# Performance work log

Hardware: AMD Instinct MI355X
Metric: run time of the kernel (lower is better)

Reference implementation:

```python
import jax, jax.numpy as jnp
import numpy as np

C = 512
NUM_GROUPS = 32
EPS = 1e-6


def setup_inputs() -> dict:
    key = jax.random.key(0)
    ks = jax.random.split(key, 10)
    B, H, W = 4, 64, 64
    scale = 1.0 / np.sqrt(C)
    return {
        "hidden_states": jax.random.normal(ks[0], (B, C, H, W), dtype=jnp.float32),
        "gn_scale": jnp.ones((C,), dtype=jnp.float32),
        "gn_bias": jnp.zeros((C,), dtype=jnp.float32),
        "wq": jax.random.normal(ks[1], (C, C), dtype=jnp.float32) * scale,
        "bq": jnp.zeros((C,), dtype=jnp.float32),
        "wk": jax.random.normal(ks[2], (C, C), dtype=jnp.float32) * scale,
        "bk": jnp.zeros((C,), dtype=jnp.float32),
        "wv": jax.random.normal(ks[3], (C, C), dtype=jnp.float32) * scale,
        "bv": jnp.zeros((C,), dtype=jnp.float32),
        "wp": jax.random.normal(ks[4], (C, C), dtype=jnp.float32) * scale,
        "bp": jnp.zeros((C,), dtype=jnp.float32),
    }


def _group_norm(x, scale, bias):
    # x: (B, C, H, W); GroupNorm(32 groups, eps=1e-6, affine)
    B, Cc, H, W = x.shape
    xg = x.reshape(B, NUM_GROUPS, Cc // NUM_GROUPS, H, W)
    mean = jnp.mean(xg, axis=(2, 3, 4), keepdims=True)
    var = jnp.var(xg, axis=(2, 3, 4), keepdims=True)
    xg = (xg - mean) * jax.lax.rsqrt(var + EPS)
    x = xg.reshape(B, Cc, H, W)
    return x * scale[None, :, None, None] + bias[None, :, None, None]


def _conv1x1(x, w, b):
    # 1x1 conv == channel matmul; x: (B,C,H,W), w: (Cout,Cin)
    return jnp.einsum('bchw,oc->bohw', x, w) + b[None, :, None, None]


def reference(hidden_states, gn_scale, gn_bias, wq, bq, wk, bk, wv, bv, wp, bp):
    residual = hidden_states
    h = _group_norm(hidden_states, gn_scale, gn_bias)
    q = _conv1x1(h, wq, bq)
    k = _conv1x1(h, wk, bk)
    v = _conv1x1(h, wv, bv)
    B, Cc, H, W = q.shape
    N = H * W
    q = q.reshape(B, Cc, N)  # (B,C,N)
    k = k.reshape(B, Cc, N)
    v = v.reshape(B, Cc, N)
    # attn[b,i,j] = softmax_j( q_i . k_j * C^-0.5 )
    attn = jnp.einsum('bci,bcj->bij', q, k) * (Cc ** -0.5)
    attn = jax.nn.softmax(attn, axis=2)
    # out[b,c,i] = sum_j v[b,c,j] * attn[b,i,j]
    out = jnp.einsum('bcj,bij->bci', v, attn)
    out = out.reshape(B, Cc, H, W)
    out = _conv1x1(out, wp, bp)
    return out + residual
```

## Files before the change

kernel.cpp:

```cpp
#include <hip/hip_runtime.h>
#include <cstdint>
#include <cstddef>


#define CDIM 512
#define NSP  4096
#define NB   4
#define M0   12.0f

using bf16x8 = __attribute__((ext_vector_type(8))) __bf16;
using f32x4  = __attribute__((ext_vector_type(4))) float;
using u16x4  = __attribute__((ext_vector_type(4))) unsigned short;
using h8     = __attribute__((ext_vector_type(8))) _Float16;

__device__ __forceinline__ unsigned short f2bf(float f) {
  unsigned int u = __float_as_uint(f);
  u += 0x7fffu + ((u >> 16) & 1u);
  return (unsigned short)(u >> 16);
}

__device__ __forceinline__ void async_copy16(const unsigned short* g, unsigned short* l) {
  __builtin_amdgcn_global_load_lds(
      (const __attribute__((address_space(1))) void*)g,
      (__attribute__((address_space(3))) void*)l, 16, 0, 0);
}

__global__ __launch_bounds__(256) void gn_stats(const float* __restrict__ x,
                                                float* __restrict__ stats) {
  const size_t base = (size_t)blockIdx.x * 65536;
  const float4* p = (const float4*)(x + base);
  float s = 0.f, ss = 0.f;
  for (int i = threadIdx.x; i < 16384; i += 256) {
    float4 v = p[i];
    s  += v.x + v.y + v.z + v.w;
    ss += v.x*v.x + v.y*v.y + v.z*v.z + v.w*v.w;
  }
  for (int off = 32; off; off >>= 1) {
    s  += __shfl_xor(s, off);
    ss += __shfl_xor(ss, off);
  }
  __shared__ float rs[4], rss[4];
  const int w = threadIdx.x >> 6;
  if ((threadIdx.x & 63) == 0) { rs[w] = s; rss[w] = ss; }
  __syncthreads();
  if (threadIdx.x == 0) {
    float S  = rs[0] + rs[1] + rs[2] + rs[3];
    float SS = rss[0] + rss[1] + rss[2] + rss[3];
    float mean = S * (1.f / 65536.f);
    float var  = SS * (1.f / 65536.f) - mean * mean;
    stats[2 * blockIdx.x]     = mean;
    stats[2 * blockIdx.x + 1] = rsqrtf(var + 1e-6f);
  }
}

__global__ __launch_bounds__(256) void norm_transpose(
    const float* __restrict__ x, const float* __restrict__ stats,
    const float* __restrict__ gns, const float* __restrict__ gnb,
    unsigned short* __restrict__ hnt) {
  __shared__ float tile[64][65];
  const int b  = blockIdx.z;
  const int c0 = blockIdx.y * 64, n0 = blockIdx.x * 64;
  const int tx = threadIdx.x & 63, ty = threadIdx.x >> 6;
  for (int i = 0; i < 16; ++i) {
    int cl = ty * 16 + i;
    int c  = c0 + cl;
    int g  = c >> 4;
    float mean = stats[(b * 32 + g) * 2];
    float rstd = stats[(b * 32 + g) * 2 + 1];
    float v = x[((size_t)(b * CDIM + c)) * NSP + n0 + tx];
    tile[cl][tx] = (v - mean) * rstd * gns[c] + gnb[c];
  }
  __syncthreads();
  for (int i = 0; i < 16; ++i) {
    int nl = ty * 16 + i;
    hnt[((size_t)(b * NSP + n0 + nl)) * CDIM + c0 + tx] = f2bf(tile[tx][nl]);
  }
}

__global__ __launch_bounds__(256) void weights_to_bf16(
    const float* __restrict__ w0, const float* __restrict__ w1,
    const float* __restrict__ w2, const float* __restrict__ w3,
    unsigned short* __restrict__ o0, unsigned short* __restrict__ o1,
    unsigned short* __restrict__ o2, unsigned short* __restrict__ o3) {
  const float* s; unsigned short* o;
  switch (blockIdx.y) {
    case 0: s = w0; o = o0; break;
    case 1: s = w1; o = o1; break;
    case 2: s = w2; o = o2; break;
    default: s = w3; o = o3; break;
  }
  int i = blockIdx.x * 256 + threadIdx.x;
  float4 v = ((const float4*)s)[i];
  u16x4 r = {f2bf(v.x), f2bf(v.y), f2bf(v.z), f2bf(v.w)};
  *(u16x4*)(o + (size_t)i * 4) = r;
}

template <int BIAS_MODE, int OUT_MODE, int RESID>
__global__ __launch_bounds__(256) void gemm_nt(
    const unsigned short* __restrict__ A, const unsigned short* __restrict__ Bt,
    void* __restrict__ Dv, const float* __restrict__ bias,
    const float* __restrict__ resid,
    int M, int N, int K, float scale, long sA, long sB, long sD, long sR) {
  __shared__ unsigned short lsA[2][128 * 32];
  __shared__ unsigned short lsB[2][128 * 32];
  const int tid = threadIdx.x;
  const int w = tid >> 6, lane = tid & 63;
  const int wr = w >> 1, wc = w & 1;
  const int b = blockIdx.z;
  const int bm0 = blockIdx.y * 128, bn0 = blockIdx.x * 128;
  const unsigned short* Ab = A + (size_t)b * sA;
  const unsigned short* Bb = Bt + (size_t)b * sB;

  f32x4 acc[4][4] = {};
  const int r0  = w * 16 + (lane >> 2);
  const int kof = (lane & 3) * 8;
  const int fr  = lane & 15, kf = (lane >> 4) * 8;

  for (int it = 0; it < 2; ++it) {
    int row = it * 64 + r0;
    async_copy16(Ab + (size_t)(bm0 + row) * K + kof, &lsA[0][row * 32 + kof]);
    async_copy16(Bb + (size_t)(bn0 + row) * K + kof, &lsB[0][row * 32 + kof]);
  }
  __syncthreads();

  int cur = 0;
  for (int k0 = 0; k0 < K; k0 += 32) {
    const int nk = k0 + 32;
    if (nk < K) {
      for (int it = 0; it < 2; ++it) {
        int row = it * 64 + r0;
        async_copy16(Ab + (size_t)(bm0 + row) * K + nk + kof, &lsA[cur ^ 1][row * 32 + kof]);
        async_copy16(Bb + (size_t)(bn0 + row) * K + nk + kof, &lsB[cur ^ 1][row * 32 + kof]);
      }
    }
    bf16x8 af[4], bff[4];
    for (int i = 0; i < 4; ++i) {
      af[i]  = *(const bf16x8*)(&lsA[cur][(wr * 64 + i * 16 + fr) * 32 + kf]);
      bff[i] = *(const bf16x8*)(&lsB[cur][(wc * 64 + i * 16 + fr) * 32 + kf]);
    }
    for (int i = 0; i < 4; ++i)
      for (int j = 0; j < 4; ++j)
        acc[i][j] = __builtin_amdgcn_mfma_f32_16x16x32_bf16(af[i], bff[j], acc[i][j], 0, 0, 0);
    __syncthreads();
    cur ^= 1;
  }

  const int col_l = lane & 15, row_l = (lane >> 4) * 4;
  for (int i = 0; i < 4; ++i)
    for (int j = 0; j < 4; ++j) {
      int gr = bm0 + wr * 64 + i * 16 + row_l;
      int gc = bn0 + wc * 64 + j * 16 + col_l;
      for (int r = 0; r < 4; ++r) {
        float v = acc[i][j][r] * scale;
        if (BIAS_MODE == 1) v += bias[gr + r];
        if (BIAS_MODE == 2) v += bias[gc];
        if (RESID) v += resid[(size_t)b * sR + (size_t)(gr + r) * N + gc];
        if (OUT_MODE == 1)
          ((unsigned short*)Dv)[(size_t)b * sD + (size_t)(gr + r) * N + gc] = f2bf(v);
        else
          ((float*)Dv)[(size_t)b * sD + (size_t)(gr + r) * N + gc] = v;
      }
    }
}

template <int OUT_MODE, int SPLITK, int EXPL>
__global__ __launch_bounds__(512, 2) void gemm256(
    const unsigned short* __restrict__ A, const unsigned short* __restrict__ Bt,
    void* __restrict__ Dv, float* __restrict__ lsum,
    int M, int N, int K, float scale, long sA, long sB, long sD, int kLen) {
  __shared__ unsigned short lsA[2][256 * 64];
  __shared__ unsigned short lsB[2][256 * 64];
  const int tid = threadIdx.x;
  const int wid = tid >> 6, lane = tid & 63;
  const int wm = wid >> 2, wn = wid & 3;
  const int fr = lane & 15, kq = lane >> 4;
  const int b = SPLITK ? (blockIdx.z & 3) : blockIdx.z;
  const int bm0 = blockIdx.y * 256, bn0 = blockIdx.x * 256;
  const unsigned short* Ab = A + (size_t)b * sA;
  const unsigned short* Bb = Bt + (size_t)b * sB;
  const size_t dOff = SPLITK ? (size_t)blockIdx.z * (size_t)M * N
                             : (size_t)b * (size_t)sD;
  const int kStart = SPLITK ? (blockIdx.z >> 2) * kLen : 0;
  const int ntiles = (SPLITK ? kLen : K) >> 6;

  const int srow = tid >> 3;
  const int schunk = (tid & 7) ^ (srow & 7);
  const int s5 = srow >> 5, sl = srow & 31;

  auto stage_part = [&](int t, int buf, int part) {
    const int k0 = kStart + t * 64;
    if (part == 0 || part == 2) {
      const int mh = part >> 1;
#pragma unroll
      for (int i = 0; i < 2; ++i) {
        const int rl = i * 128 + mh * 64 + srow;
        async_copy16(Ab + (size_t)(bm0 + rl) * K + k0 + schunk * 8,
                     &lsA[buf][rl * 64 + (tid & 7) * 8]);
      }
    } else {
      const int nh = part >> 1;
#pragma unroll
      for (int i = 0; i < 2; ++i) {
        const int rl = i * 128 + s5 * 64 + nh * 32 + sl;
        async_copy16(Bb + (size_t)(bn0 + rl) * K + k0 + schunk * 8,
                     &lsB[buf][rl * 64 + (tid & 7) * 8]);
      }
    }
  };

  f32x4 acc[8][4] = {};
  const int cko0 = (((0 * 4 + kq) ^ (fr & 7)) * 8);
  const int cko1 = (((1 * 4 + kq) ^ (fr & 7)) * 8);
  const int arow = wm * 128 + fr;
  const int brow = wn * 64 + fr;

  stage_part(0, 0, 0); stage_part(0, 0, 1);
  stage_part(0, 0, 3); stage_part(0, 0, 2);

  for (int t = 0; t < ntiles; ++t) {
    const int cur = t & 1, nbuf = cur ^ 1;
    const unsigned short* la = &lsA[cur][0];
    const unsigned short* lb = &lsB[cur][0];
    const bool pre = (t + 1 < ntiles);

    bf16x8 bgr[4][2];
    bf16x8 af[4][2];

    asm volatile("s_waitcnt vmcnt(2)\n\ts_barrier" ::: "memory");
    if (pre) { stage_part(t + 1, nbuf, 0); stage_part(t + 1, nbuf, 1); }
#pragma unroll
    for (int j = 0; j < 4; ++j) {
      const int rb = (brow + j * 16) * 64;
      bgr[j][0] = *(const bf16x8*)&lb[rb + cko0];
      bgr[j][1] = *(const bf16x8*)&lb[rb + cko1];
    }
#pragma unroll
    for (int i = 0; i < 4; ++i) {
      const int ra = (arow + i * 16) * 64;
      af[i][0] = *(const bf16x8*)&la[ra + cko0];
      af[i][1] = *(const bf16x8*)&la[ra + cko1];
    }
    __builtin_amdgcn_s_setprio(1);
#pragma unroll
    for (int i = 0; i < 4; ++i)
#pragma unroll
      for (int j = 0; j < 4; ++j) {
        acc[i][j] = __builtin_amdgcn_mfma_f32_16x16x32_bf16(af[i][0], bgr[j][0], acc[i][j], 0, 0, 0);
        acc[i][j] = __builtin_amdgcn_mfma_f32_16x16x32_bf16(af[i][1], bgr[j][1], acc[i][j], 0, 0, 0);
      }
    __builtin_amdgcn_s_setprio(0);

    if (pre) asm volatile("s_waitcnt vmcnt(4)\n\ts_barrier" ::: "memory");
    else     asm volatile("s_waitcnt vmcnt(0)\n\ts_barrier" ::: "memory");
    if (pre) { stage_part(t + 1, nbuf, 3); stage_part(t + 1, nbuf, 2); }
#pragma unroll
    for (int i = 0; i < 4; ++i) {
      const int ra = (arow + 64 + i * 16) * 64;
      af[i][0] = *(const bf16x8*)&la[ra + cko0];
      af[i][1] = *(const bf16x8*)&la[ra + cko1];
    }
    __builtin_amdgcn_s_setprio(1);
#pragma unroll
    for (int i = 0; i < 4; ++i)
#pragma unroll
      for (int j = 0; j < 4; ++j) {
        acc[4 + i][j] = __builtin_amdgcn_mfma_f32_16x16x32_bf16(af[i][0], bgr[j][0], acc[4 + i][j], 0, 0, 0);
        acc[4 + i][j] = __builtin_amdgcn_mfma_f32_16x16x32_bf16(af[i][1], bgr[j][1], acc[4 + i][j], 0, 0, 0);
      }
    __builtin_amdgcn_s_setprio(0);
  }

  float rs[8][4];
  if (EXPL)
#pragma unroll
    for (int i = 0; i < 8; ++i)
#pragma unroll
      for (int r = 0; r < 4; ++r) rs[i][r] = 0.f;

#pragma unroll
  for (int mi = 0; mi < 8; ++mi)
#pragma unroll
    for (int ni = 0; ni < 4; ++ni) {
      const int gr = bm0 + wm * 128 + mi * 16 + kq * 4;
      const int gc = bn0 + wn * 64 + ni * 16 + fr;
#pragma unroll
      for (int r = 0; r < 4; ++r) {
        float v;
        if (EXPL) {
          v = __expf(fmaf(acc[mi][ni][r], scale, -M0));
          rs[mi][r] += v;
        } else {
          v = acc[mi][ni][r] * scale;
        }
        if (OUT_MODE == 1)
          ((unsigned short*)Dv)[dOff + (size_t)(gr + r) * N + gc] = f2bf(v);
        else
          ((_Float16*)Dv)[dOff + (size_t)(gr + r) * N + gc] = (_Float16)v;
      }
    }

  if (EXPL) {
#pragma unroll
    for (int mi = 0; mi < 8; ++mi)
#pragma unroll
      for (int r = 0; r < 4; ++r) {
        float v = rs[mi][r];
        v += __shfl_xor(v, 1); v += __shfl_xor(v, 2);
        v += __shfl_xor(v, 4); v += __shfl_xor(v, 8);
        if (fr == 0) {
          int gr = bm0 + wm * 128 + mi * 16 + kq * 4 + r;
          atomicAdd(&lsum[(size_t)b * M + gr], v);
        }
      }
  }
}

__global__ __launch_bounds__(256) void reduce_div(const _Float16* __restrict__ Op,
                                                  const float* __restrict__ l,
                                                  unsigned short* __restrict__ ot) {
  const size_t stride = (size_t)NB * NSP * CDIM;
  size_t base = ((size_t)blockIdx.x * 256 + threadIdx.x) * 8;
  float linv = 1.f / l[base >> 9];
  h8 a = *(const h8*)(Op + base);
  h8 c = *(const h8*)(Op + stride + base);
  u16x4 o0, o1;
#pragma unroll
  for (int i = 0; i < 4; ++i) {
    o0[i] = f2bf(((float)a[i] + (float)c[i]) * linv);
    o1[i] = f2bf(((float)a[i + 4] + (float)c[i + 4]) * linv);
  }
  *(u16x4*)(ot + base) = o0;
  *(u16x4*)(ot + base + 4) = o1;
}

extern "C" void kernel_launch(void* const* d_in, const int* in_sizes, int n_in,
                              void* d_out, int out_size, void* d_ws, size_t ws_size,
                              hipStream_t stream) {
  const float* hs  = (const float*)d_in[0];
  const float* gns = (const float*)d_in[1];
  const float* gnb = (const float*)d_in[2];
  const float* wq  = (const float*)d_in[3];
  const float* bq  = (const float*)d_in[4];
  const float* wk  = (const float*)d_in[5];
  const float* bk  = (const float*)d_in[6];
  const float* wv  = (const float*)d_in[7];
  const float* bv  = (const float*)d_in[8];
  const float* wp  = (const float*)d_in[9];
  const float* bp  = (const float*)d_in[10];

  char* p = (char*)d_ws;
  unsigned short* wqb = (unsigned short*)p; p += (size_t)CDIM * CDIM * 2;
  unsigned short* wkb = (unsigned short*)p; p += (size_t)CDIM * CDIM * 2;
  unsigned short* wvb = (unsigned short*)p; p += (size_t)CDIM * CDIM * 2;
  unsigned short* wpb = (unsigned short*)p; p += (size_t)CDIM * CDIM * 2;
  const size_t bn = (size_t)NSP * CDIM;
  unsigned short* hnt = (unsigned short*)p; p += NB * bn * 2;
  unsigned short* qt  = (unsigned short*)p; p += NB * bn * 2;
  unsigned short* kt  = (unsigned short*)p; p += NB * bn * 2;
  unsigned short* vcn = (unsigned short*)p; p += NB * bn * 2;
  unsigned short* P   = (unsigned short*)p; p += (size_t)NB * NSP * NSP * 2;
  _Float16* Op = (_Float16*)p;  p += (size_t)2 * NB * bn * 2;
  float* lsum  = (float*)p;     p += (size_t)NB * NSP * 4;
  float* stats = (float*)p;     p += 256 * 4;
  unsigned short* ot = hnt;

  hipMemsetAsync(lsum, 0, (size_t)NB * NSP * 4, stream);
  weights_to_bf16<<<dim3(256, 4), 256, 0, stream>>>(wq, wk, wv, wp, wqb, wkb, wvb, wpb);
  gn_stats<<<128, 256, 0, stream>>>(hs, stats);
  norm_transpose<<<dim3(64, 8, 4), 256, 0, stream>>>(hs, stats, gns, gnb, hnt);

  const long sBN = (long)bn;
  const long sPP = (long)NSP * NSP;
  gemm_nt<2, 1, 0><<<dim3(4, 32, NB), 256, 0, stream>>>(
      hnt, wqb, qt, bq, nullptr, NSP, CDIM, CDIM, 1.f, sBN, 0, sBN, 0);
  gemm_nt<2, 1, 0><<<dim3(4, 32, NB), 256, 0, stream>>>(
      hnt, wkb, kt, bk, nullptr, NSP, CDIM, CDIM, 1.f, sBN, 0, sBN, 0);
  gemm_nt<1, 1, 0><<<dim3(32, 4, NB), 256, 0, stream>>>(
      wvb, hnt, vcn, bv, nullptr, CDIM, NSP, CDIM, 1.f, 0, sBN, sBN, 0);

  const float sc = 0.044194173824159216f;
  gemm256<1, 0, 1><<<dim3(16, 16, NB), 512, 0, stream>>>(
      qt, kt, P, lsum, NSP, NSP, CDIM, sc, sBN, sBN, sPP, 0);

  gemm256<2, 1, 0><<<dim3(2, 16, 2 * NB), 512, 0, stream>>>(
      P, vcn, Op, nullptr, NSP, CDIM, NSP, 1.f, sPP, sBN, 0, NSP / 2);

  reduce_div<<<4096, 256, 0, stream>>>(Op, lsum, ot);

  gemm_nt<1, 0, 1><<<dim3(32, 4, NB), 256, 0, stream>>>(
      wpb, ot, (float*)d_out, bp, hs, CDIM, NSP, CDIM, 1.f, 0, sBN, sBN, sBN);
}
```

Baseline: 336.3 us.

## Split GEMM k-tile into four ping-pong quadrant phases with barriers

Restructures the main GEMM loop so each k-tile runs as four 8-MFMA quadrant phases. Each phase's LDS fragment loads and one next-tile staging part are bracketed by barriers, so wavegroups interleave loads and math more finely and B fragments are split into two halves. This aims to overlap global-to-LDS copies with MFMA work and cut register pressure. The cost is more barriers per tile and waitcnt accounting that is fragile and could stall or race if the counts are wrong.

```diff
diff --git a/kernel.cpp b/kernel.cpp
--- a/kernel.cpp
+++ b/kernel.cpp
@@ -214,61 +214,81 @@
   const int arow = wm * 128 + fr;
   const int brow = wn * 64 + fr;
 
+#define MMA8(AF, BG, MO, NO)                                                  \
+  __builtin_amdgcn_s_setprio(1);                                              \
+  _Pragma("unroll")                                                           \
+  for (int i = 0; i < 4; ++i)                                                 \
+    _Pragma("unroll")                                                         \
+    for (int j = 0; j < 2; ++j) {                                             \
+      acc[(MO) + i][(NO) + j] = __builtin_amdgcn_mfma_f32_16x16x32_bf16(      \
+          AF[i][0], BG[j][0], acc[(MO) + i][(NO) + j], 0, 0, 0);              \
+      acc[(MO) + i][(NO) + j] = __builtin_amdgcn_mfma_f32_16x16x32_bf16(      \
+          AF[i][1], BG[j][1], acc[(MO) + i][(NO) + j], 0, 0, 0);              \
+    }                                                                         \
+  __builtin_amdgcn_s_setprio(0);
+
   stage_part(0, 0, 0); stage_part(0, 0, 1);
-  stage_part(0, 0, 3); stage_part(0, 0, 2);
+  stage_part(0, 0, 2); stage_part(0, 0, 3);
+  asm volatile("s_waitcnt vmcnt(4)\n\ts_barrier" ::: "memory");
 
   for (int t = 0; t < ntiles; ++t) {
     const int cur = t & 1, nbuf = cur ^ 1;
     const unsigned short* la = &lsA[cur][0];
     const unsigned short* lb = &lsB[cur][0];
     const bool pre = (t + 1 < ntiles);
-
-    bf16x8 bgr[4][2];
-    bf16x8 af[4][2];
-
-    asm volatile("s_waitcnt vmcnt(2)\n\ts_barrier" ::: "memory");
-    if (pre) { stage_part(t + 1, nbuf, 0); stage_part(t + 1, nbuf, 1); }
-#pragma unroll
-    for (int j = 0; j < 4; ++j) {
-      const int rb = (brow + j * 16) * 64;
-      bgr[j][0] = *(const bf16x8*)&lb[rb + cko0];
-      bgr[j][1] = *(const bf16x8*)&lb[rb + cko1];
-    }
+    bf16x8 af0[4][2], af1[4][2], bg0[2][2], bg1[2][2];
+
+    asm volatile("s_waitcnt vmcnt(2)" ::: "memory");
 #pragma unroll
     for (int i = 0; i < 4; ++i) {
       const int ra = (arow + i * 16) * 64;
-      af[i][0] = *(const bf16x8*)&la[ra + cko0];
-      af[i][1] = *(const bf16x8*)&la[ra + cko1];
-    }
-    __builtin_amdgcn_s_setprio(1);
-#pragma unroll
-    for (int i = 0; i < 4; ++i)
-#pragma unroll
-      for (int j = 0; j < 4; ++j) {
-        acc[i][j] = __builtin_amdgcn_mfma_f32_16x16x32_bf16(af[i][0], bgr[j][0], acc[i][j], 0, 0, 0);
-        acc[i][j] = __builtin_amdgcn_mfma_f32_16x16x32_bf16(af[i][1], bgr[j][1], acc[i][j], 0, 0, 0);
-      }
-    __builtin_amdgcn_s_setprio(0);
-
-    if (pre) asm volatile("s_waitcnt vmcnt(4)\n\ts_barrier" ::: "memory");
-    else     asm volatile("s_waitcnt vmcnt(0)\n\ts_barrier" ::: "memory");
-    if (pre) { stage_part(t + 1, nbuf, 3); stage_part(t + 1, nbuf, 2); }
+      af0[i][0] = *(const bf16x8*)&la[ra + cko0];
+      af0[i][1] = *(const bf16x8*)&la[ra + cko1];
+    }
+#pragma unroll
+    for (int j = 0; j < 2; ++j) {
+      const int rb = (brow + j * 16) * 64;
+      bg0[j][0] = *(const bf16x8*)&lb[rb + cko0];
+      bg0[j][1] = *(const bf16x8*)&lb[rb + cko1];
+    }
+    if (pre) stage_part(t + 1, nbuf, 0);
+    asm volatile("s_barrier" ::: "memory");
+    MMA8(af0, bg0, 0, 0)
+    asm volatile("s_barrier" ::: "memory");
+
+    if (pre) asm volatile("s_waitcnt vmcnt(2)" ::: "memory");
+    else     asm volatile("s_waitcnt vmcnt(0)" ::: "memory");
 #pragma unroll
     for (int i = 0; i < 4; ++i) {
       const int ra = (arow + 64 + i * 16) * 64;
-      af[i][0] = *(const bf16x8*)&la[ra + cko0];
-      af[i][1] = *(const bf16x8*)&la[ra + cko1];
-    }
-    __builtin_amdgcn_s_setprio(1);
-#pragma unroll
-    for (int i = 0; i < 4; ++i)
-#pragma unroll
-      for (int j = 0; j < 4; ++j) {
-        acc[4 + i][j] = __builtin_amdgcn_mfma_f32_16x16x32_bf16(af[i][0], bgr[j][0], acc[4 + i][j], 0, 0, 0);
-        acc[4 + i][j] = __builtin_amdgcn_mfma_f32_16x16x32_bf16(af[i][1], bgr[j][1], acc[4 + i][j], 0, 0, 0);
-      }
-    __builtin_amdgcn_s_setprio(0);
-  }
+      af1[i][0] = *(const bf16x8*)&la[ra + cko0];
+      af1[i][1] = *(const bf16x8*)&la[ra + cko1];
+    }
+    if (pre) stage_part(t + 1, nbuf, 1);
+    asm volatile("s_barrier" ::: "memory");
+    MMA8(af1, bg0, 4, 0)
+    asm volatile("s_barrier" ::: "memory");
+
+#pragma unroll
+    for (int j = 0; j < 2; ++j) {
+      const int rb = (brow + 32 + j * 16) * 64;
+      bg1[j][0] = *(const bf16x8*)&lb[rb + cko0];
+      bg1[j][1] = *(const bf16x8*)&lb[rb + cko1];
+    }
+    if (pre) stage_part(t + 1, nbuf, 2);
+    asm volatile("s_barrier" ::: "memory");
+    MMA8(af1, bg1, 4, 2)
+    asm volatile("s_barrier" ::: "memory");
+
+    if (pre) {
+      asm volatile("s_waitcnt vmcnt(2)" ::: "memory");
+      stage_part(t + 1, nbuf, 3);
+    }
+    asm volatile("s_barrier" ::: "memory");
+    MMA8(af0, bg1, 0, 2)
+    asm volatile("s_barrier" ::: "memory");
+  }
+#undef MMA8
 
   float rs[8][4];
   if (EXPL)
```

Measured after the change: 318.3 us. -5.3%, faster.
